# Kernel optimization log

Hardware: AMD Instinct MI355X
Metric: run time of the kernel (lower is better)

## Reference

```python
import jax, jax.numpy as jnp
import numpy as np

B, C, H, W = 8, 512, 32, 32
NUM_HEADS = 8
NUM_GROUPS = 32
EPS = 1e-5


def setup_inputs() -> dict:
    key = jax.random.key(0)
    k1, k2, k3 = jax.random.split(key, 3)
    x = jax.random.normal(k1, (B, C, H, W), dtype=jnp.float32)
    gn_w = jnp.ones((C,), dtype=jnp.float32)
    gn_b = jnp.zeros((C,), dtype=jnp.float32)
    qkv_w = jax.random.normal(k2, (3 * C, C), dtype=jnp.float32) * 0.02
    qkv_b = jnp.zeros((3 * C,), dtype=jnp.float32)
    # NOTE: original zero-initializes proj_out; we use random weights so the
    # residual branch is non-trivial for correctness testing.
    proj_w = jax.random.normal(k3, (C, C), dtype=jnp.float32) * 0.02
    proj_b = jnp.zeros((C,), dtype=jnp.float32)
    return {"x": x, "gn_w": gn_w, "gn_b": gn_b, "qkv_w": qkv_w,
            "qkv_b": qkv_b, "proj_w": proj_w, "proj_b": proj_b}


def _group_norm(x, w, b):
    # x: [B, C, T]
    Bn, Cn, T = x.shape
    xg = x.reshape(Bn, NUM_GROUPS, Cn // NUM_GROUPS, T)
    mean = xg.mean(axis=(2, 3), keepdims=True)
    var = xg.var(axis=(2, 3), keepdims=True)
    xn = ((xg - mean) * jax.lax.rsqrt(var + EPS)).reshape(Bn, Cn, T)
    return xn * w[None, :, None] + b[None, :, None]


def reference(x, gn_w, gn_b, qkv_w, qkv_b, proj_w, proj_b):
    b, c = x.shape[0], x.shape[1]
    spatial = x.shape[2:]
    xr = x.reshape(b, c, -1)                      # [B, C, T]
    xn = _group_norm(xr, gn_w, gn_b)
    # 1x1 conv1d: [3C, C] x [B, C, T] -> [B, 3C, T]
    qkv = jnp.einsum('oc,bct->bot', qkv_w, xn) + qkv_b[None, :, None]
    T = qkv.shape[-1]
    qkv = qkv.reshape(b * NUM_HEADS, -1, T)       # [B*Nh, 3*ch, T]
    ch = qkv.shape[1] // 3
    q, k, v = jnp.split(qkv, 3, axis=1)
    scale = 1.0 / np.sqrt(np.sqrt(ch))
    weight = jnp.einsum('bct,bcs->bts', q * scale, k * scale)  # [B*Nh, T, T]
    weight = jax.nn.softmax(weight.astype(jnp.float32), axis=-1).astype(weight.dtype)
    h = jnp.einsum('bts,bcs->bct', weight, v)     # [B*Nh, ch, T]
    h = h.reshape(b, c, T)
    h = jnp.einsum('oc,bct->bot', proj_w, h) + proj_b[None, :, None]
    return (xr + h).reshape(b, c, *spatial)
```

## Files before the change

kernel.cpp:

```cpp
#include <hip/hip_runtime.h>
#include <math.h>

#define Bn 8
#define Cn 512
#define Tn 1024

typedef __attribute__((ext_vector_type(8))) short bf16x8;
typedef __attribute__((ext_vector_type(4))) float f32x4;

__device__ __forceinline__ unsigned short f2bf(float f) {
  unsigned int u = __builtin_bit_cast(unsigned int, f);
  u = (u + 0x7FFFu + ((u >> 16) & 1u)) >> 16;
  return (unsigned short)u;
}

__device__ __forceinline__ unsigned int cvtpk_bf16(float lo, float hi) {
  unsigned int r;
  asm("v_cvt_pk_bf16_f32 %0, %1, %2" : "=v"(r) : "v"(lo), "v"(hi));
  return r;
}

typedef __attribute__((address_space(1))) const unsigned int GU32;
typedef __attribute__((address_space(3))) unsigned int LU32;
__device__ __forceinline__ void gld16(const unsigned short* g, unsigned short* l) {
  __builtin_amdgcn_global_load_lds((GU32*)g, (LU32*)l, 16, 0, 0);
}

__device__ __forceinline__ void stage128x64(const unsigned short* __restrict__ src,
                                            size_t row_stride, unsigned short* lds, int tid) {
  const int w = tid >> 6;
  const int row = tid >> 3;
  const int sc = (tid & 7) ^ ((tid >> 3) & 7);
#pragma unroll
  for (int c = 0; c < 4; ++c)
    gld16(src + (size_t)(c * 32 + row) * row_stride + sc * 8,
          (unsigned short*)((char*)lds + c * 4096 + w * 1024));
}

__device__ __forceinline__ void stage64x64(const unsigned short* __restrict__ src,
                                           size_t row_stride, unsigned short* lds, int tid) {
  const int w = tid >> 6;
  const int row = tid >> 3;
  const int sc = (tid & 7) ^ ((tid >> 3) & 7);
#pragma unroll
  for (int c = 0; c < 2; ++c)
    gld16(src + (size_t)(c * 32 + row) * row_stride + sc * 8,
          (unsigned short*)((char*)lds + c * 4096 + w * 1024));
}

__global__ __launch_bounds__(256) void gn_kernel(const float* __restrict__ x,
                                                 const float* __restrict__ gw,
                                                 const float* __restrict__ gb,
                                                 unsigned short* __restrict__ xn_t) {
  const int blk = blockIdx.x;
  const int b = blk >> 5, g = blk & 31;
  const size_t base = ((size_t)b * Cn + (size_t)g * 16) * Tn;
  const float4* __restrict__ xin = (const float4*)(x + base);
  const int tid = threadIdx.x;

  float vv[16][4];
  float sum = 0.f, sq = 0.f;
#pragma unroll
  for (int k = 0; k < 16; ++k) {
    const float4 t4 = xin[tid + (k << 8)];
    vv[k][0] = t4.x; vv[k][1] = t4.y; vv[k][2] = t4.z; vv[k][3] = t4.w;
    sum += t4.x + t4.y + t4.z + t4.w;
    sq += t4.x * t4.x + t4.y * t4.y + t4.z * t4.z + t4.w * t4.w;
  }

  __shared__ float rs[8];
  const int lane = tid & 63, wv = tid >> 6;
#pragma unroll
  for (int off = 32; off > 0; off >>= 1) {
    sum += __shfl_down(sum, off);
    sq += __shfl_down(sq, off);
  }
  if (lane == 0) { rs[wv] = sum; rs[4 + wv] = sq; }
  __syncthreads();
  const float ts = rs[0] + rs[1] + rs[2] + rs[3];
  const float tq = rs[4] + rs[5] + rs[6] + rs[7];
  const float mean = ts * (1.f / 16384.f);
  const float var = tq * (1.f / 16384.f) - mean * mean;
  const float rstd = rsqrtf(var + 1e-5f);

  float aa[16], bb[16];
#pragma unroll
  for (int k = 0; k < 16; ++k) {
    aa[k] = rstd * gw[g * 16 + k];
    bb[k] = gb[g * 16 + k] - mean * aa[k];
  }

#pragma unroll
  for (int j = 0; j < 4; ++j) {
    const int t = tid * 4 + j;
    unsigned int pk[8];
#pragma unroll
    for (int k2 = 0; k2 < 8; ++k2) {
      const unsigned int lo = f2bf(vv[2 * k2][j] * aa[2 * k2] + bb[2 * k2]);
      const unsigned int hi = f2bf(vv[2 * k2 + 1][j] * aa[2 * k2 + 1] + bb[2 * k2 + 1]);
      pk[k2] = lo | (hi << 16);
    }
    unsigned short* dst = xn_t + ((size_t)(b * Tn + t)) * Cn + g * 16;
    *(uint4*)dst = make_uint4(pk[0], pk[1], pk[2], pk[3]);
    *((uint4*)dst + 1) = make_uint4(pk[4], pk[5], pk[6], pk[7]);
  }
}

__global__ __launch_bounds__(256) void cvt2_kernel(const float* __restrict__ qkv_w,
                                                   const float* __restrict__ proj_w,
                                                   unsigned short* __restrict__ wqkv,
                                                   unsigned short* __restrict__ wproj) {
  const int blk = blockIdx.x;
  const float* src = (blk < 768) ? qkv_w : proj_w;
  unsigned short* dst = (blk < 768) ? wqkv : wproj;
  const int i = ((blk < 768) ? blk : blk - 768) * 256 + threadIdx.x;
  const float4 f = ((const float4*)src)[i];
  uint2 o;
  o.x = (unsigned int)f2bf(f.x) | ((unsigned int)f2bf(f.y) << 16);
  o.y = (unsigned int)f2bf(f.z) | ((unsigned int)f2bf(f.w) << 16);
  ((uint2*)dst)[i] = o;
}

__global__ __launch_bounds__(256, 2) void qkv_gemm(const unsigned short* __restrict__ Wb,
                                                   const unsigned short* __restrict__ Xb,
                                                   const float* __restrict__ bias,
                                                   unsigned short* __restrict__ q_t,
                                                   unsigned short* __restrict__ k_t,
                                                   unsigned short* __restrict__ v_t) {
  __shared__ unsigned short As[2][8192];
  __shared__ unsigned short Bs[2][8192];
  const int id = blockIdx.x;
  const int b = id & 7;
  const int inner = id >> 3;
  const int bx = inner % 12, by = inner / 12;
  const int o0 = bx * 128, t0 = by * 128;
  const int tid = threadIdx.x, lane = tid & 63, w = tid >> 6;
  const int wr = w >> 1, wc = w & 1;
  const int ln = lane & 15, g16 = lane >> 4;
  const unsigned short* __restrict__ X = Xb + (size_t)b * Tn * Cn;
  const unsigned short* __restrict__ Wt = Wb + (size_t)o0 * 512;
  const unsigned short* __restrict__ Xt = X + (size_t)t0 * 512;

  f32x4 acc[4][4];
#pragma unroll
  for (int mt = 0; mt < 4; ++mt)
#pragma unroll
    for (int nt = 0; nt < 4; ++nt) acc[mt][nt] = (f32x4){0.f, 0.f, 0.f, 0.f};

  stage128x64(Wt, 512, &As[0][0], tid);
  stage128x64(Xt, 512, &Bs[0][0], tid);
  __syncthreads();

  int buf = 0;
  for (int k0 = 0; k0 < 512; k0 += 64) {
    if (k0 + 64 < 512) {
      stage128x64(Wt + k0 + 64, 512, &As[buf ^ 1][0], tid);
      stage128x64(Xt + k0 + 64, 512, &Bs[buf ^ 1][0], tid);
    }
    const char* Ab = (const char*)&As[buf][0];
    const char* Bb = (const char*)&Bs[buf][0];
    bf16x8 af[4][2], bfr[4][2];
#pragma unroll
    for (int mt = 0; mt < 4; ++mt)
#pragma unroll
      for (int kk = 0; kk < 2; ++kk) {
        const int row = wr * 64 + mt * 16 + ln;
        const int c16 = ((kk << 2) | g16) ^ (ln & 7);
        af[mt][kk] = *(const bf16x8*)(Ab + row * 128 + (c16 << 4));
      }
#pragma unroll
    for (int nt = 0; nt < 4; ++nt)
#pragma unroll
      for (int kk = 0; kk < 2; ++kk) {
        const int row = wc * 64 + nt * 16 + ln;
        const int c16 = ((kk << 2) | g16) ^ (ln & 7);
        bfr[nt][kk] = *(const bf16x8*)(Bb + row * 128 + (c16 << 4));
      }
#pragma unroll
    for (int kk = 0; kk < 2; ++kk)
#pragma unroll
      for (int mt = 0; mt < 4; ++mt)
#pragma unroll
        for (int nt = 0; nt < 4; ++nt)
          acc[mt][nt] =
              __builtin_amdgcn_mfma_f32_16x16x32_bf16(af[mt][kk], bfr[nt][kk], acc[mt][nt], 0, 0, 0);
    __syncthreads();
    buf ^= 1;
  }

  const int o_base = o0 + wr * 64, t_base = t0 + wc * 64;
  const int partw = (o_base >> 6) % 3;
  const int bh = b * 8 + o_base / 192;
  unsigned short (*Vlds)[136] = (unsigned short (*)[136])(&As[0][0]);

  if (partw < 2) {
    unsigned short* qk = (partw == 0 ? q_t : k_t) + (size_t)bh * 65536;
    const float sc = (partw == 0) ? 0.18033688f : 1.0f;
#pragma unroll
    for (int mt = 0; mt < 4; ++mt) {
      const int ob16 = o_base + mt * 16;
      float bv[4];
#pragma unroll
      for (int r = 0; r < 4; ++r) bv[r] = bias[ob16 + g16 * 4 + r];
#pragma unroll
      for (int nt = 0; nt < 4; ++nt) {
        const int t = t_base + nt * 16 + ln;
        const float v0 = (acc[mt][nt][0] + bv[0]) * sc;
        const float v1 = (acc[mt][nt][1] + bv[1]) * sc;
        const float v2 = (acc[mt][nt][2] + bv[2]) * sc;
        const float v3 = (acc[mt][nt][3] + bv[3]) * sc;
        uint2 pk;
        pk.x = (unsigned int)f2bf(v0) | ((unsigned int)f2bf(v1) << 16);
        pk.y = (unsigned int)f2bf(v2) | ((unsigned int)f2bf(v3) << 16);
        *(uint2*)(qk + (size_t)t * 64 + mt * 16 + g16 * 4) = pk;
      }
    }
  } else {
#pragma unroll
    for (int mt = 0; mt < 4; ++mt) {
      float bv[4];
#pragma unroll
      for (int r = 0; r < 4; ++r) bv[r] = bias[o_base + mt * 16 + g16 * 4 + r];
#pragma unroll
      for (int nt = 0; nt < 4; ++nt)
#pragma unroll
        for (int r = 0; r < 4; ++r)
          Vlds[mt * 16 + g16 * 4 + r][wc * 64 + nt * 16 + ln] = f2bf(acc[mt][nt][r] + bv[r]);
    }
  }
  __syncthreads();
  const int bxm = bx % 3;
  if (bxm) {
    const int o_first = o0 + (bxm - 1) * 64;
    unsigned short* vdst = v_t + (size_t)(b * 8 + o_first / 192) * 65536;
    const int c = tid >> 2, tseg = (tid & 3) << 5;
    const unsigned short* src = &Vlds[c][tseg];
    unsigned short* p = vdst + (size_t)c * Tn + t0 + tseg;
    const uint4 d0 = *(const uint4*)(src);
    const uint4 d1 = *(const uint4*)(src + 8);
    const uint4 d2 = *(const uint4*)(src + 16);
    const uint4 d3 = *(const uint4*)(src + 24);
    *(uint4*)(p) = d0;
    *(uint4*)(p + 8) = d1;
    *(uint4*)(p + 16) = d2;
    *(uint4*)(p + 24) = d3;
  }
}

__global__ __launch_bounds__(256, 2) void attn_kernel(const unsigned short* __restrict__ q_t,
                                                      const unsigned short* __restrict__ k_t,
                                                      const unsigned short* __restrict__ v_t,
                                                      unsigned short* __restrict__ h_t) {
  __shared__ unsigned short Ks[2][4096];
  __shared__ unsigned short Vs[2][4096];
  __shared__ __align__(16) unsigned short P_lds[4][2048];
  const int id = blockIdx.x;
  const int xcd = id & 7, qq = id >> 3;
  const int b = qq >> 3, tc = qq & 7;
  const int bh = b * 8 + xcd;
  const int tid = threadIdx.x, lane = tid & 63, w = tid >> 6;
  const int t_wave = tc * 128 + w * 32;
  const int ln = lane & 15, g16 = lane >> 4, g8 = g16 * 8;
  const unsigned short* __restrict__ qbase = q_t + (size_t)bh * 65536;
  const unsigned short* __restrict__ kbase = k_t + (size_t)bh * 65536;
  const unsigned short* __restrict__ vbase = v_t + (size_t)bh * 65536;
  char* __restrict__ Pb = (char*)P_lds[w];

  int koff[4][2];
#pragma unroll
  for (int f = 0; f < 4; ++f)
#pragma unroll
    for (int kb = 0; kb < 2; ++kb)
      koff[f][kb] = (f * 16 + ln) * 128 + ((((kb << 2) | g16) ^ (ln & 7)) << 4);

  int wr_off[4], rd_off[2];
#pragma unroll
  for (int ns = 0; ns < 4; ++ns)
    wr_off[ns] = ln * 128 + ((((ns << 1) | (g16 >> 1)) ^ (ln & 7)) << 4) + ((g16 & 1) << 3);
#pragma unroll
  for (int kb = 0; kb < 2; ++kb)
    rd_off[kb] = ln * 128 + ((((kb << 2) | g16) ^ (ln & 7)) << 4);

  bf16x8 qf[2][2];
#pragma unroll
  for (int mt = 0; mt < 2; ++mt)
#pragma unroll
    for (int kb = 0; kb < 2; ++kb)
      qf[mt][kb] = *(const bf16x8*)(qbase + (size_t)(t_wave + mt * 16 + ln) * 64 + kb * 32 + g8);

  f32x4 o_acc[2][4];
#pragma unroll
  for (int mt = 0; mt < 2; ++mt)
#pragma unroll
    for (int nc = 0; nc < 4; ++nc) o_acc[mt][nc] = (f32x4){0.f, 0.f, 0.f, 0.f};
  float m_run[2] = {-1e30f, -1e30f}, l_run[2] = {0.f, 0.f};

  stage64x64(kbase, 64, &Ks[0][0], tid);
  stage64x64(vbase, 1024, &Vs[0][0], tid);
  __syncthreads();

  int buf = 0;
  for (int st = 0; st < 16; ++st) {
    const int s0 = st << 6;
    if (st < 15) {
      stage64x64(kbase + (size_t)(s0 + 64) * 64, 64, &Ks[buf ^ 1][0], tid);
      stage64x64(vbase + (s0 + 64), 1024, &Vs[buf ^ 1][0], tid);
    }
    const char* Kb = (const char*)&Ks[buf][0];
    const char* Vb = (const char*)&Vs[buf][0];

    bf16x8 kf[4][2];
#pragma unroll
    for (int ns = 0; ns < 4; ++ns)
#pragma unroll
      for (int kb = 0; kb < 2; ++kb)
        kf[ns][kb] = *(const bf16x8*)(Kb + koff[ns][kb]);

    f32x4 sacc[2][4];
#pragma unroll
    for (int mt = 0; mt < 2; ++mt)
#pragma unroll
      for (int ns = 0; ns < 4; ++ns) sacc[mt][ns] = (f32x4){0.f, 0.f, 0.f, 0.f};

    __builtin_amdgcn_s_setprio(1);
#pragma unroll
    for (int kb = 0; kb < 2; ++kb)
#pragma unroll
      for (int ns = 0; ns < 4; ++ns) {
        sacc[0][ns] = __builtin_amdgcn_mfma_f32_16x16x32_bf16(kf[ns][kb], qf[0][kb], sacc[0][ns], 0, 0, 0);
        sacc[1][ns] = __builtin_amdgcn_mfma_f32_16x16x32_bf16(kf[ns][kb], qf[1][kb], sacc[1][ns], 0, 0, 0);
      }
    __builtin_amdgcn_s_setprio(0);

    float m[2];
#pragma unroll
    for (int mt = 0; mt < 2; ++mt) {
      float mm = sacc[mt][0][0];
#pragma unroll
      for (int ns = 0; ns < 4; ++ns)
#pragma unroll
        for (int r = 0; r < 4; ++r) mm = fmaxf(mm, sacc[mt][ns][r]);
      mm = fmaxf(mm, __shfl_xor(mm, 16));
      mm = fmaxf(mm, __shfl_xor(mm, 32));
      m[mt] = mm;
    }

    const bool need = (m[0] > m_run[0] + 11.f) || (m[1] > m_run[1] + 11.f);
    if (__any(need ? 1 : 0)) {
#pragma unroll
      for (int mt = 0; mt < 2; ++mt) {
        const float mnew = fmaxf(m_run[mt], m[mt]);
        const float al = __builtin_amdgcn_exp2f(m_run[mt] - mnew);
        m_run[mt] = mnew;
        l_run[mt] *= al;
        float al4[4];
#pragma unroll
        for (int r = 0; r < 4; ++r) al4[r] = __shfl(al, (g16 << 2) + r);
#pragma unroll
        for (int nc = 0; nc < 4; ++nc)
#pragma unroll
          for (int r = 0; r < 4; ++r) o_acc[mt][nc][r] *= al4[r];
      }
    }

#pragma unroll
    for (int mt = 0; mt < 2; ++mt) {
      float rsum = 0.f;
#pragma unroll
      for (int ns = 0; ns < 4; ++ns) {
#pragma unroll
        for (int r = 0; r < 4; ++r) {
          sacc[mt][ns][r] = __builtin_amdgcn_exp2f(sacc[mt][ns][r] - m_run[mt]);
          rsum += sacc[mt][ns][r];
        }
      }
      rsum += __shfl_xor(rsum, 16);
      rsum += __shfl_xor(rsum, 32);
      l_run[mt] += rsum;
#pragma unroll
      for (int ns = 0; ns < 4; ++ns) {
        uint2 pk2;
        pk2.x = cvtpk_bf16(sacc[mt][ns][0], sacc[mt][ns][1]);
        pk2.y = cvtpk_bf16(sacc[mt][ns][2], sacc[mt][ns][3]);
        *(uint2*)(Pb + mt * 2048 + wr_off[ns]) = pk2;
      }
    }

    bf16x8 pf[2][2];
#pragma unroll
    for (int mt = 0; mt < 2; ++mt)
#pragma unroll
      for (int kb = 0; kb < 2; ++kb)
        pf[mt][kb] = *(const bf16x8*)(Pb + mt * 2048 + rd_off[kb]);

    bf16x8 vf[4][2];
#pragma unroll
    for (int nc = 0; nc < 4; ++nc)
#pragma unroll
      for (int kb = 0; kb < 2; ++kb)
        vf[nc][kb] = *(const bf16x8*)(Vb + koff[nc][kb]);

    __builtin_amdgcn_s_setprio(1);
#pragma unroll
    for (int kb = 0; kb < 2; ++kb)
#pragma unroll
      for (int nc = 0; nc < 4; ++nc) {
        o_acc[0][nc] = __builtin_amdgcn_mfma_f32_16x16x32_bf16(pf[0][kb], vf[nc][kb], o_acc[0][nc], 0, 0, 0);
        o_acc[1][nc] = __builtin_amdgcn_mfma_f32_16x16x32_bf16(pf[1][kb], vf[nc][kb], o_acc[1][nc], 0, 0, 0);
      }
    __builtin_amdgcn_s_setprio(0);

    __syncthreads();
    buf ^= 1;
  }

  const int bb = bh >> 3, hh = bh & 7;
  unsigned short* __restrict__ hb = h_t + (size_t)bb * Tn * Cn + hh * 64;
#pragma unroll
  for (int mt = 0; mt < 2; ++mt) {
    const float rl = 1.f / l_run[mt];
    float rl4[4];
#pragma unroll
    for (int r = 0; r < 4; ++r) rl4[r] = __shfl(rl, (g16 << 2) + r);
#pragma unroll
    for (int nc = 0; nc < 4; ++nc) {
      const int c = nc * 16 + ln;
#pragma unroll
      for (int r = 0; r < 4; ++r) {
        const int t = t_wave + mt * 16 + g16 * 4 + r;
        hb[(size_t)t * Cn + c] = f2bf(o_acc[mt][nc][r] * rl4[r]);
      }
    }
  }
}

__global__ __launch_bounds__(256, 2) void proj_gemm(const unsigned short* __restrict__ Wb,
                                                    const unsigned short* __restrict__ Hb,
                                                    const float* __restrict__ pbias,
                                                    const float* __restrict__ x,
                                                    float* __restrict__ out) {
  __shared__ unsigned short As[2][8192];
  __shared__ unsigned short Bs[2][8192];
  const int id = blockIdx.x;
  const int b = id & 7;
  const int inner = id >> 3;
  const int bx = inner & 3, by = inner >> 2;
  const int o0 = bx * 128, t0 = by * 128;
  const int tid = threadIdx.x, lane = tid & 63, w = tid >> 6;
  const int wr = w >> 1, wc = w & 1;
  const int ln = lane & 15, g16 = lane >> 4;
  const unsigned short* __restrict__ H = Hb + (size_t)b * Tn * Cn;
  const unsigned short* __restrict__ Wt = Wb + (size_t)o0 * 512;
  const unsigned short* __restrict__ Ht = H + (size_t)t0 * 512;

  f32x4 acc[4][4];
#pragma unroll
  for (int mt = 0; mt < 4; ++mt)
#pragma unroll
    for (int nt = 0; nt < 4; ++nt) acc[mt][nt] = (f32x4){0.f, 0.f, 0.f, 0.f};

  stage128x64(Wt, 512, &As[0][0], tid);
  stage128x64(Ht, 512, &Bs[0][0], tid);
  __syncthreads();

  int buf = 0;
  for (int k0 = 0; k0 < 512; k0 += 64) {
    if (k0 + 64 < 512) {
      stage128x64(Wt + k0 + 64, 512, &As[buf ^ 1][0], tid);
      stage128x64(Ht + k0 + 64, 512, &Bs[buf ^ 1][0], tid);
    }
    const char* Ab = (const char*)&As[buf][0];
    const char* Bb = (const char*)&Bs[buf][0];
    bf16x8 af[4][2], bfr[4][2];
#pragma unroll
    for (int mt = 0; mt < 4; ++mt)
#pragma unroll
      for (int kk = 0; kk < 2; ++kk) {
        const int row = wr * 64 + mt * 16 + ln;
        const int c16 = ((kk << 2) | g16) ^ (ln & 7);
        af[mt][kk] = *(const bf16x8*)(Ab + row * 128 + (c16 << 4));
      }
#pragma unroll
    for (int nt = 0; nt < 4; ++nt)
#pragma unroll
      for (int kk = 0; kk < 2; ++kk) {
        const int row = wc * 64 + nt * 16 + ln;
        const int c16 = ((kk << 2) | g16) ^ (ln & 7);
        bfr[nt][kk] = *(const bf16x8*)(Bb + row * 128 + (c16 << 4));
      }
#pragma unroll
    for (int kk = 0; kk < 2; ++kk)
#pragma unroll
      for (int mt = 0; mt < 4; ++mt)
#pragma unroll
        for (int nt = 0; nt < 4; ++nt)
          acc[mt][nt] =
              __builtin_amdgcn_mfma_f32_16x16x32_bf16(af[mt][kk], bfr[nt][kk], acc[mt][nt], 0, 0, 0);
    __syncthreads();
    buf ^= 1;
  }

  const int o_base = o0 + wr * 64, t_base = t0 + wc * 64;
#pragma unroll
  for (int mt = 0; mt < 4; ++mt) {
    const int ob = o_base + mt * 16 + g16 * 4;
    float pb[4];
#pragma unroll
    for (int r = 0; r < 4; ++r) pb[r] = pbias[ob + r];
#pragma unroll
    for (int nt = 0; nt < 4; ++nt) {
      const int t = t_base + nt * 16 + ln;
#pragma unroll
      for (int r = 0; r < 4; ++r) {
        const size_t idx = (size_t)b * Cn * Tn + (size_t)(ob + r) * Tn + t;
        out[idx] = acc[mt][nt][r] + pb[r] + x[idx];
      }
    }
  }
}

extern "C" void kernel_launch(void* const* d_in, const int* in_sizes, int n_in,
                              void* d_out, int out_size, void* d_ws, size_t ws_size,
                              hipStream_t stream) {
  (void)in_sizes; (void)n_in; (void)out_size; (void)ws_size;
  const float* x = (const float*)d_in[0];
  const float* gn_w = (const float*)d_in[1];
  const float* gn_b = (const float*)d_in[2];
  const float* qkv_w = (const float*)d_in[3];
  const float* qkv_b = (const float*)d_in[4];
  const float* proj_w = (const float*)d_in[5];
  const float* proj_b = (const float*)d_in[6];
  float* out = (float*)d_out;

  unsigned short* wsu = (unsigned short*)d_ws;
  unsigned short* xn_t = wsu;
  unsigned short* wqkv = xn_t + (size_t)4194304;
  unsigned short* wproj = wqkv + (size_t)786432;
  unsigned short* q_t = wproj + (size_t)262144;
  unsigned short* k_t = q_t + (size_t)4194304;
  unsigned short* v_t = k_t + (size_t)4194304;
  unsigned short* h_t = v_t + (size_t)4194304;

  gn_kernel<<<dim3(256), 256, 0, stream>>>(x, gn_w, gn_b, xn_t);
  cvt2_kernel<<<dim3(1024), 256, 0, stream>>>(qkv_w, proj_w, wqkv, wproj);
  qkv_gemm<<<dim3(768), 256, 0, stream>>>(wqkv, xn_t, qkv_b, q_t, k_t, v_t);
  attn_kernel<<<dim3(512), 256, 0, stream>>>(q_t, k_t, v_t, h_t);
  proj_gemm<<<dim3(256), 256, 0, stream>>>(wproj, h_t, proj_b, x, out);
}
```

Baseline: 154.8 us.

## Triple-buffer attention K/V staging and merge groupnorm with weight conversion kernel

The attention kernel moves from double to triple-buffered K/V tiles in LDS. It prefetches two tiles ahead and waits with explicit vmcnt counts instead of a full __syncthreads drain, so global loads overlap more compute. Separately, the groupnorm and weight-conversion kernels become one launch, removing a kernel boundary. The cost is extra LDS per block, which could lower occupancy, and fragile hand-tuned waitcnt values.

```diff
diff --git a/kernel.cpp b/kernel.cpp
--- a/kernel.cpp
+++ b/kernel.cpp
@@ -48,15 +48,32 @@
           (unsigned short*)((char*)lds + c * 4096 + w * 1024));
 }
 
-__global__ __launch_bounds__(256) void gn_kernel(const float* __restrict__ x,
-                                                 const float* __restrict__ gw,
-                                                 const float* __restrict__ gb,
-                                                 unsigned short* __restrict__ xn_t) {
+__global__ __launch_bounds__(256) void prep_kernel(const float* __restrict__ x,
+                                                   const float* __restrict__ gw,
+                                                   const float* __restrict__ gb,
+                                                   unsigned short* __restrict__ xn_t,
+                                                   const float* __restrict__ qkv_w,
+                                                   const float* __restrict__ proj_w,
+                                                   unsigned short* __restrict__ wqkv,
+                                                   unsigned short* __restrict__ wproj) {
+  const int tid = threadIdx.x;
+  if (blockIdx.x >= 256) {
+    const int blk = blockIdx.x - 256;
+    const float* src = (blk < 768) ? qkv_w : proj_w;
+    unsigned short* dst = (blk < 768) ? wqkv : wproj;
+    const int i = ((blk < 768) ? blk : blk - 768) * 256 + tid;
+    const float4 f = ((const float4*)src)[i];
+    uint2 o;
+    o.x = (unsigned int)f2bf(f.x) | ((unsigned int)f2bf(f.y) << 16);
+    o.y = (unsigned int)f2bf(f.z) | ((unsigned int)f2bf(f.w) << 16);
+    ((uint2*)dst)[i] = o;
+    return;
+  }
+
   const int blk = blockIdx.x;
   const int b = blk >> 5, g = blk & 31;
   const size_t base = ((size_t)b * Cn + (size_t)g * 16) * Tn;
   const float4* __restrict__ xin = (const float4*)(x + base);
-  const int tid = threadIdx.x;
 
   float vv[16][4];
   float sum = 0.f, sq = 0.f;
@@ -104,21 +121,6 @@
     *(uint4*)dst = make_uint4(pk[0], pk[1], pk[2], pk[3]);
     *((uint4*)dst + 1) = make_uint4(pk[4], pk[5], pk[6], pk[7]);
   }
-}
-
-__global__ __launch_bounds__(256) void cvt2_kernel(const float* __restrict__ qkv_w,
-                                                   const float* __restrict__ proj_w,
-                                                   unsigned short* __restrict__ wqkv,
-                                                   unsigned short* __restrict__ wproj) {
-  const int blk = blockIdx.x;
-  const float* src = (blk < 768) ? qkv_w : proj_w;
-  unsigned short* dst = (blk < 768) ? wqkv : wproj;
-  const int i = ((blk < 768) ? blk : blk - 768) * 256 + threadIdx.x;
-  const float4 f = ((const float4*)src)[i];
-  uint2 o;
-  o.x = (unsigned int)f2bf(f.x) | ((unsigned int)f2bf(f.y) << 16);
-  o.y = (unsigned int)f2bf(f.z) | ((unsigned int)f2bf(f.w) << 16);
-  ((uint2*)dst)[i] = o;
 }
 
 __global__ __launch_bounds__(256, 2) void qkv_gemm(const unsigned short* __restrict__ Wb,
@@ -251,8 +253,8 @@
                                                       const unsigned short* __restrict__ k_t,
                                                       const unsigned short* __restrict__ v_t,
                                                       unsigned short* __restrict__ h_t) {
-  __shared__ unsigned short Ks[2][4096];
-  __shared__ unsigned short Vs[2][4096];
+  __shared__ unsigned short Ks[3][4096];
+  __shared__ unsigned short Vs[3][4096];
   __shared__ __align__(16) unsigned short P_lds[4][2048];
   const int id = blockIdx.x;
   const int xcd = id & 7, qq = id >> 3;
@@ -297,17 +299,22 @@
 
   stage64x64(kbase, 64, &Ks[0][0], tid);
   stage64x64(vbase, 1024, &Vs[0][0], tid);
-  __syncthreads();
-
-  int buf = 0;
+  stage64x64(kbase + (size_t)64 * 64, 64, &Ks[1][0], tid);
+  stage64x64(vbase + 64, 1024, &Vs[1][0], tid);
+  asm volatile("s_waitcnt vmcnt(4)" ::: "memory");
+  __builtin_amdgcn_s_barrier();
+  __builtin_amdgcn_sched_barrier(0);
+
+  int cur = 0;
   for (int st = 0; st < 16; ++st) {
-    const int s0 = st << 6;
-    if (st < 15) {
-      stage64x64(kbase + (size_t)(s0 + 64) * 64, 64, &Ks[buf ^ 1][0], tid);
-      stage64x64(vbase + (s0 + 64), 1024, &Vs[buf ^ 1][0], tid);
-    }
-    const char* Kb = (const char*)&Ks[buf][0];
-    const char* Vb = (const char*)&Vs[buf][0];
+    const int s2 = (cur >= 1) ? cur - 1 : cur + 2;
+    if (st < 14) {
+      const int s0n = (st + 2) << 6;
+      stage64x64(kbase + (size_t)s0n * 64, 64, &Ks[s2][0], tid);
+      stage64x64(vbase + s0n, 1024, &Vs[s2][0], tid);
+    }
+    const char* Kb = (const char*)&Ks[cur][0];
+    const char* Vb = (const char*)&Vs[cur][0];
 
     bf16x8 kf[4][2];
 #pragma unroll
@@ -410,8 +417,14 @@
       }
     __builtin_amdgcn_s_setprio(0);
 
-    __syncthreads();
-    buf ^= 1;
+    if (st < 14) {
+      asm volatile("s_waitcnt vmcnt(4)" ::: "memory");
+    } else {
+      asm volatile("s_waitcnt vmcnt(0)" ::: "memory");
+    }
+    __builtin_amdgcn_s_barrier();
+    __builtin_amdgcn_sched_barrier(0);
+    cur = (cur >= 2) ? 0 : cur + 1;
   }
 
   const int bb = bh >> 3, hh = bh & 7;
@@ -541,8 +554,7 @@
   unsigned short* v_t = k_t + (size_t)4194304;
   unsigned short* h_t = v_t + (size_t)4194304;
 
-  gn_kernel<<<dim3(256), 256, 0, stream>>>(x, gn_w, gn_b, xn_t);
-  cvt2_kernel<<<dim3(1024), 256, 0, stream>>>(qkv_w, proj_w, wqkv, wproj);
+  prep_kernel<<<dim3(1280), 256, 0, stream>>>(x, gn_w, gn_b, xn_t, qkv_w, proj_w, wqkv, wproj);
   qkv_gemm<<<dim3(768), 256, 0, stream>>>(wqkv, xn_t, qkv_b, q_t, k_t, v_t);
   attn_kernel<<<dim3(512), 256, 0, stream>>>(q_t, k_t, v_t, h_t);
   proj_gemm<<<dim3(256), 256, 0, stream>>>(wproj, h_t, proj_b, x, out);
```

Measured after the change: 153.7 us. Within noise of the previous version (-0.7%).
